# Kernel optimization log

Measured on AMD Instinct MI355X. Metric: run time of the kernel, lower is better.

The kernel has to match this reference:

```python
import jax, jax.numpy as jnp
import numpy as np


def setup_inputs() -> dict:
    key = jax.random.key(0)
    k1, k2, k3, k4 = jax.random.split(key, 4)
    B, N, F, H, O = 4, 2048, 256, 8, 256
    nodes = jax.random.normal(k1, (B, N, F), dtype=jnp.float32)
    W_heads = jax.random.normal(k2, (H, F, F), dtype=jnp.float32) * (1.0 / np.sqrt(F))
    W_out = jax.random.normal(k3, (H * F, O), dtype=jnp.float32) * (1.0 / np.sqrt(H * F))
    bias = jax.random.normal(k4, (O,), dtype=jnp.float32) * 0.02
    return {"nodes": nodes, "W_heads": W_heads, "W_out": W_out, "bias": bias}


def reference(nodes, W_heads, W_out, bias):
    # nodes: [B,N,F]; W_heads: [H,F,F]; W_out: [H*F,O]; bias: [O]
    B, N, F = nodes.shape
    H = W_heads.shape[0]
    norm = 1.0 / jnp.sqrt(jnp.asarray(F, dtype=nodes.dtype))
    # per-head bilinear scores: (x @ W_h) @ x^T  -> [B,H,N,N]
    xw = jnp.einsum('bnf,hfg->bhng', nodes, W_heads)
    scores = jnp.einsum('bhng,bmg->bhnm', xw, nodes) * norm
    att = jax.nn.softmax(scores, axis=-1)
    # messages: att @ x (V = input nodes) -> [B,H,N,F]
    msgs = jnp.einsum('bhnm,bmf->bhnf', att, nodes)
    # concat heads along feature axis (head 0 first) -> [B,N,H*F]
    msgs = msgs.transpose(0, 2, 1, 3).reshape(B, N, H * F)
    return jnp.matmul(msgs, W_out) + bias
```

## Files before the change

### kernel.cpp

```cpp
#include <hip/hip_runtime.h>
#include <hip/hip_bf16.h>

#define B_ 4
#define N_ 2048
#define F_ 256
#define H_ 8
#define O_ 256

#define SCALE_QK 0.09016844005556021f

typedef __attribute__((ext_vector_type(8))) short short8;
typedef __attribute__((ext_vector_type(4))) short s16x4;
typedef __attribute__((ext_vector_type(4))) float f32x4;
typedef __attribute__((ext_vector_type(4))) unsigned int u32x4;

static __device__ __forceinline__ float bf2f(short u) {
    unsigned int x = ((unsigned int)(unsigned short)u) << 16;
    return __builtin_bit_cast(float, x);
}
static __device__ __forceinline__ short f2bf(float f) {
    unsigned int x = __builtin_bit_cast(unsigned int, f);
    unsigned int lsb = (x >> 16) & 1u;
    x += 0x7fffu + lsb;
    return (short)(x >> 16);
}
static __device__ __forceinline__ unsigned int pkbf(float a, float b) {
    return (unsigned int)(unsigned short)f2bf(a) |
           ((unsigned int)(unsigned short)f2bf(b) << 16);
}

static __device__ __forceinline__ void gld16(const short* g, short* l) {
    __builtin_amdgcn_global_load_lds(
        (const __attribute__((address_space(1))) void*)g,
        (__attribute__((address_space(3))) void*)l, 16, 0, 0);
}

__global__ __launch_bounds__(256) void cvtT_kernel(const float* __restrict__ src,
                                                   short* __restrict__ dstT,
                                                   short* __restrict__ dst2,
                                                   int R, int C) {
    __shared__ short tile[32][33];
    src  += (size_t)blockIdx.z * R * C;
    dstT += (size_t)blockIdx.z * R * C;
    if (dst2) dst2 += (size_t)blockIdx.z * R * C;
    int tx = threadIdx.x, ty = threadIdx.y;
    int c0 = blockIdx.x * 32, r0 = blockIdx.y * 32;
#pragma unroll
    for (int j = 0; j < 4; j++) {
        int r = r0 + ty + j * 8;
        short v = f2bf(src[(size_t)r * C + c0 + tx]);
        tile[ty + j * 8][tx] = v;
        if (dst2) dst2[(size_t)r * C + c0 + tx] = v;
    }
    __syncthreads();
#pragma unroll
    for (int j = 0; j < 4; j++) {
        int c = c0 + ty + j * 8;
        dstT[(size_t)c * R + r0 + tx] = tile[tx][ty + j * 8];
    }
}

__global__ __launch_bounds__(256) void cvt_kernel(const float* __restrict__ src,
                                                  short* __restrict__ dst, int n) {
    int i = blockIdx.x * 256 + threadIdx.x;
    if (i < n) dst[i] = f2bf(src[i]);
}

template <int NCT>
__device__ __forceinline__ void gemm64_bt(const short* __restrict__ A, int lda,
                                          const short* __restrict__ Bt, int ldb,
                                          float* __restrict__ C, int ldc,
                                          int K, const short* __restrict__ bias) {
    __shared__ short sA[64][72];
    __shared__ short sB[NCT * 16][72];
    int tid = threadIdx.x;
    int w = tid >> 6, l = tid & 63, lq = l & 15, quad = l >> 4;
    f32x4 acc[NCT];
#pragma unroll
    for (int i = 0; i < NCT; i++) acc[i] = (f32x4)(0.f);

    for (int kb = 0; kb < K; kb += 64) {
        __syncthreads();
#pragma unroll
        for (int i = 0; i < 2; i++) {
            int idx = tid + i * 256; int r = idx >> 3, c = (idx & 7) * 8;
            *(short8*)&sA[r][c] = *(const short8*)&A[(size_t)r * lda + kb + c];
        }
#pragma unroll
        for (int i = 0; i < NCT / 2; i++) {
            int idx = tid + i * 256; int r = idx >> 3, c = (idx & 7) * 8;
            *(short8*)&sB[r][c] = *(const short8*)&Bt[(size_t)r * ldb + kb + c];
        }
        __syncthreads();
#pragma unroll
        for (int kk = 0; kk < 2; kk++) {
            short8 af = *(const short8*)&sA[w * 16 + lq][kk * 32 + quad * 8];
#pragma unroll
            for (int ct = 0; ct < NCT; ct++) {
                short8 bf = *(const short8*)&sB[ct * 16 + lq][kk * 32 + quad * 8];
                acc[ct] = __builtin_amdgcn_mfma_f32_16x16x32_bf16(af, bf, acc[ct], 0, 0, 0);
            }
        }
    }
#pragma unroll
    for (int ct = 0; ct < NCT; ct++) {
        int col = ct * 16 + lq;
        float bv = bias ? bf2f(bias[col]) : 0.f;
#pragma unroll
        for (int r = 0; r < 4; r++) {
            int row = w * 16 + quad * 4 + r;
            C[(size_t)row * ldc + col] = acc[ct][r] + bv;
        }
    }
}

__global__ __launch_bounds__(256) void out_kernel(const short* __restrict__ msgs,
                                                  const short* __restrict__ WoutT,
                                                  const short* __restrict__ bias,
                                                  float* __restrict__ out) {
    int mt = blockIdx.x, nt = blockIdx.y;
    gemm64_bt<4>(msgs + (size_t)mt * 64 * (H_ * F_), H_ * F_,
                 WoutT + (size_t)nt * 64 * (H_ * F_), H_ * F_,
                 out + (size_t)mt * 64 * O_ + nt * 64, O_,
                 H_ * F_, bias + nt * 64);
}


#define STAGE_KV(KT, KVF, KVTF) do {                                         \
    _Pragma("unroll")                                                        \
    for (int i_ = 0; i_ < 4; i_++) {                                         \
        int rk_ = w * 8 + i_ * 2 + (l >> 5);                                 \
        int bk_ = (l & 31) ^ (rk_ & 31);                                     \
        gld16(&Xb[(size_t)((KT) * 64 + rk_) * F_ + bk_ * 8],                 \
              &KVF[(w * 8 + i_ * 2) * 256]);                                 \
        int rt_ = w * 32 + i_ * 8 + (l >> 3);                                \
        int bt_ = (l & 7) ^ (rt_ & 7);                                       \
        gld16(&XTb[(size_t)rt_ * N_ + (KT) * 64 + bt_ * 8],                  \
              &KVTF[(w * 32 + i_ * 8) * 64]);                                \
    }                                                                        \
} while (0)

#define COMPUTE_KT(KVF, KVTF) do {                                           \
    f32x4 sacc[4];                                                           \
    _Pragma("unroll")                                                        \
    for (int ct = 0; ct < 4; ct++) sacc[ct] = (f32x4)(0.f);                  \
    __builtin_amdgcn_s_setprio(1);                                           \
    _Pragma("unroll")                                                        \
    for (int kk = 0; kk < 8; kk++) {                                         \
        _Pragma("unroll")                                                    \
        for (int ct = 0; ct < 4; ct++) {                                     \
            int arow = ct * 16 + lq;                                         \
            int ab = (kk * 4 + quad) ^ (arow & 31);                          \
            short8 af = *(const short8*)&KVF[arow * 256 + ab * 8];           \
            sacc[ct] = __builtin_amdgcn_mfma_f32_16x16x32_bf16(af, aq[kk], sacc[ct], 0, 0, 0); \
        }                                                                    \
    }                                                                        \
    __builtin_amdgcn_s_setprio(0);                                           \
    float mx = -INFINITY;                                                    \
    _Pragma("unroll")                                                        \
    for (int ct = 0; ct < 4; ct++)                                           \
        _Pragma("unroll")                                                    \
        for (int r_ = 0; r_ < 4; r_++) mx = fmaxf(mx, sacc[ct][r_]);         \
    mx = fmaxf(mx, __shfl_xor(mx, 16));                                      \
    mx = fmaxf(mx, __shfl_xor(mx, 32));                                      \
    float mn = fmaxf(m_q, mx);                                               \
    float alpha = exp2f(m_q - mn);                                           \
    m_q = mn;                                                                \
    float pv[4][4]; float s_ = 0.f;                                          \
    _Pragma("unroll")                                                        \
    for (int ct = 0; ct < 4; ct++)                                           \
        _Pragma("unroll")                                                    \
        for (int r_ = 0; r_ < 4; r_++) {                                     \
            pv[ct][r_] = exp2f(sacc[ct][r_] - mn);                           \
            s_ += pv[ct][r_];                                                \
        }                                                                    \
    s_ += __shfl_xor(s_, 16);                                                \
    s_ += __shfl_xor(s_, 32);                                                \
    l_q = l_q * alpha + s_;                                                  \
    if (!__all(alpha == 1.0f)) {                                             \
        _Pragma("unroll")                                                    \
        for (int ct = 0; ct < 16; ct++)                                      \
            _Pragma("unroll")                                                \
            for (int r_ = 0; r_ < 4; r_++) oacc[ct][r_] *= alpha;            \
    }                                                                        \
    unsigned int w2[4][2];                                                   \
    _Pragma("unroll")                                                        \
    for (int ct = 0; ct < 4; ct++) {                                         \
        w2[ct][0] = pkbf(pv[ct][0], pv[ct][1]);                              \
        w2[ct][1] = pkbf(pv[ct][2], pv[ct][3]);                              \
    }                                                                        \
    int sl0 = (2 * (quad & 1)) * 16 + lq;                                    \
    int sl1 = sl0 + 16;                                                      \
    bool hi = (quad >> 1) != 0;                                              \
    short8 pfrag[2];                                                         \
    _Pragma("unroll")                                                        \
    for (int kk = 0; kk < 2; kk++) {                                         \
        unsigned int u0 = __shfl((int)w2[2 * kk][0], sl0);                   \
        unsigned int u1 = __shfl((int)w2[2 * kk][1], sl0);                   \
        unsigned int u2 = __shfl((int)w2[2 * kk][0], sl1);                   \
        unsigned int u3 = __shfl((int)w2[2 * kk][1], sl1);                   \
        unsigned int v0 = __shfl((int)w2[2 * kk + 1][0], sl0);               \
        unsigned int v1 = __shfl((int)w2[2 * kk + 1][1], sl0);               \
        unsigned int v2 = __shfl((int)w2[2 * kk + 1][0], sl1);               \
        unsigned int v3 = __shfl((int)w2[2 * kk + 1][1], sl1);               \
        u32x4 pk = { hi ? v0 : u0, hi ? v1 : u1, hi ? v2 : u2, hi ? v3 : u3 }; \
        pfrag[kk] = __builtin_bit_cast(short8, pk);                          \
    }                                                                        \
    __builtin_amdgcn_s_setprio(1);                                           \
    _Pragma("unroll")                                                        \
    for (int ct = 0; ct < 16; ct++) {                                        \
        int arow = ct * 16 + lq;                                             \
        short8 a0 = *(const short8*)&KVTF[arow * 64 + ((quad) ^ (arow & 7)) * 8]; \
        short8 a1 = *(const short8*)&KVTF[arow * 64 + ((4 + quad) ^ (arow & 7)) * 8]; \
        oacc[ct] = __builtin_amdgcn_mfma_f32_16x16x32_bf16(a0, pfrag[0], oacc[ct], 0, 0, 0); \
        oacc[ct] = __builtin_amdgcn_mfma_f32_16x16x32_bf16(a1, pfrag[1], oacc[ct], 0, 0, 0); \
    }                                                                        \
    __builtin_amdgcn_s_setprio(0);                                           \
} while (0)

__global__ __launch_bounds__(512) void attn_kernel(const short* __restrict__ X,
                                                   const short* __restrict__ WhT,
                                                   const short* __restrict__ XT,
                                                   short* __restrict__ msgs) {
    __shared__ short kvfA[64 * 256];
    __shared__ short kvfB[64 * 256];
    __shared__ short kvTfA[256 * 64];
    __shared__ short kvTfB[256 * 64];

    int qt = blockIdx.x, bh = blockIdx.y, b = bh >> 3, h = bh & 7;
    int tid = threadIdx.x, w = tid >> 6, l = tid & 63, lq = l & 15, quad = l >> 4;
    int q0 = qt * 128;

    const short* Xb  = X  + (size_t)b * N_ * F_;
    const short* XTb = XT + (size_t)b * F_ * N_;
    const short* Whh = WhT + (size_t)h * F_ * F_;

    f32x4 oacc[16];
    short8 aq[8];

#pragma unroll
    for (int i = 0; i < 16; i++) oacc[i] = (f32x4)(0.f);
    {
        short* xdst = (w < 4) ? kvfA : kvfB;
        int wl = w & 3;
#pragma unroll
        for (int i = 0; i < 8; i++) {
            int r = wl * 16 + i * 2 + (l >> 5);
            int bb = (l & 31) ^ (r & 31);
            gld16(&Xb[(size_t)(q0 + ((w >> 2) * 64) + r) * F_ + bb * 8],
                  &xdst[(wl * 16 + i * 2) * 256]);
        }
    }
    const short* xsrc = (w < 4) ? kvfA : kvfB;
#pragma unroll 1
    for (int kb = 0; kb < 4; kb++) {
        __syncthreads();
#pragma unroll
        for (int i = 0; i < 4; i++) {
            int rt = w * 32 + i * 8 + (l >> 3);
            int bt = (l & 7) ^ (rt & 7);
            gld16(&Whh[(size_t)rt * F_ + kb * 64 + bt * 8], &kvTfA[(w * 32 + i * 8) * 64]);
        }
        __syncthreads();
#pragma unroll
        for (int kk = 0; kk < 2; kk++) {
            int arow = (w & 3) * 16 + lq;
            int ab = (kb * 8 + kk * 4 + quad) ^ (arow & 31);
            short8 af = *(const short8*)&xsrc[arow * 256 + ab * 8];
#pragma unroll
            for (int ct = 0; ct < 16; ct++) {
                int brow = ct * 16 + lq;
                int bb = (kk * 4 + quad) ^ (brow & 7);
                short8 bf = *(const short8*)&kvTfA[brow * 64 + bb * 8];
                oacc[ct] = __builtin_amdgcn_mfma_f32_16x16x32_bf16(af, bf, oacc[ct], 0, 0, 0);
            }
        }
    }
    __syncthreads();
    {
        short* qdst = (w < 4) ? kvTfA : kvTfB;
#pragma unroll
        for (int ct = 0; ct < 16; ct++) {
#pragma unroll
            for (int r = 0; r < 4; r++) {
                int row = (w & 3) * 16 + quad * 4 + r;
                int col = ct * 16 + lq;
                int pb = (col >> 3) ^ (row & 31);
                qdst[row * 256 + pb * 8 + (col & 7)] = f2bf(oacc[ct][r] * SCALE_QK);
            }
        }
        __syncthreads();
#pragma unroll
        for (int kk = 0; kk < 8; kk++) {
            int row = (w & 3) * 16 + lq;
            int ab = (kk * 4 + quad) ^ (row & 31);
            aq[kk] = *(const short8*)&qdst[row * 256 + ab * 8];
        }
    }
    __syncthreads();

#pragma unroll
    for (int i = 0; i < 16; i++) oacc[i] = (f32x4)(0.f);
    float m_q = -INFINITY, l_q = 0.f;

    STAGE_KV(0, kvfA, kvTfA);

#pragma unroll 1
    for (int kt = 0; kt < 32; kt++) {
        const short* KVF  = (kt & 1) ? kvfB  : kvfA;
        const short* KVTF = (kt & 1) ? kvTfB : kvTfA;
        short* nKVF  = (kt & 1) ? kvfA  : kvfB;
        short* nKVTF = (kt & 1) ? kvTfA : kvTfB;
        STAGE_KV((kt + 1) & 31, nKVF, nKVTF);
        asm volatile("s_waitcnt vmcnt(8)" ::: "memory");
        __builtin_amdgcn_sched_barrier(0);
        __builtin_amdgcn_s_barrier();
        __builtin_amdgcn_sched_barrier(0);
        COMPUTE_KT(KVF, KVTF);
        __builtin_amdgcn_sched_barrier(0);
        __builtin_amdgcn_s_barrier();
        __builtin_amdgcn_sched_barrier(0);
    }

    float inv = 1.f / l_q;
    short* Mout = msgs + (size_t)(b * N_ + q0 + w * 16 + lq) * (H_ * F_) + h * F_;
#pragma unroll
    for (int ct = 0; ct < 16; ct++) {
        s16x4 v4 = { f2bf(oacc[ct][0] * inv), f2bf(oacc[ct][1] * inv),
                     f2bf(oacc[ct][2] * inv), f2bf(oacc[ct][3] * inv) };
        *(s16x4*)&Mout[ct * 16 + quad * 4] = v4;
    }
}

extern "C" void kernel_launch(void* const* d_in, const int* in_sizes, int n_in,
                              void* d_out, int out_size, void* d_ws, size_t ws_size,
                              hipStream_t stream) {
    const float* nodes = (const float*)d_in[0];
    const float* Wh    = (const float*)d_in[1];
    const float* Wout  = (const float*)d_in[2];
    const float* bias  = (const float*)d_in[3];
    float* out = (float*)d_out;

    char* ws = (char*)d_ws;
    short* msgs   = (short*)(ws);
    short* WhT    = (short*)(ws + 33554432);
    short* WoutT  = (short*)(ws + 34603008);
    short* XT     = (short*)(ws + 35651584);
    short* Xbf    = (short*)(ws + 39845888);
    short* biasbf = (short*)(ws + 44040192);

    dim3 tblk(32, 8, 1);
    hipLaunchKernelGGL(cvtT_kernel, dim3(8, 8, 8),  tblk, 0, stream, Wh,    WhT,   (short*)nullptr, 256,  256);
    hipLaunchKernelGGL(cvtT_kernel, dim3(8, 64, 1), tblk, 0, stream, Wout,  WoutT, (short*)nullptr, 2048, 256);
    hipLaunchKernelGGL(cvtT_kernel, dim3(8, 64, 4), tblk, 0, stream, nodes, XT,    Xbf,             2048, 256);
    hipLaunchKernelGGL(cvt_kernel,  dim3(1),    dim3(256), 0, stream, bias, biasbf, 256);

    hipLaunchKernelGGL(attn_kernel, dim3(16, 32), dim3(512), 0, stream, Xbf, WhT, XT, msgs);
    hipLaunchKernelGGL(out_kernel,  dim3(128, 4), dim3(256), 0, stream, msgs, WoutT, biasbf, out);
}
```

Measured before the change: 343.5 us.

## Lazy softmax rescaling, hardware bf16 pack, and unrolled double-buffer loop

The online softmax now skips the running-max update and the rescale of the output accumulator unless some row's max grows by more than 8 (in log2 units). The deferred rescale is intended to be safe as long as exponents stay bounded. Manual round-to-nearest bf16 packing is replaced by the v_cvt_pk_bf16_f32 instruction. The KV loop is unrolled by two with fixed A/B buffers and plain __syncthreads, dropping the explicit vmcnt waits and sched barriers. This removes pointer selection and per-iteration rescale work, but it relies on __syncthreads to drain the async global-to-LDS loads, which changes how loads overlap with compute.

```diff
diff --git a/kernel.cpp b/kernel.cpp
--- a/kernel.cpp
+++ b/kernel.cpp
@@ -24,9 +24,10 @@
     x += 0x7fffu + lsb;
     return (short)(x >> 16);
 }
-static __device__ __forceinline__ unsigned int pkbf(float a, float b) {
-    return (unsigned int)(unsigned short)f2bf(a) |
-           ((unsigned int)(unsigned short)f2bf(b) << 16);
+static __device__ __forceinline__ unsigned int cvtpk(float a, float b) {
+    unsigned int r;
+    asm("v_cvt_pk_bf16_f32 %0, %1, %2" : "=v"(r) : "v"(a), "v"(b));
+    return r;
 }
 
 static __device__ __forceinline__ void gld16(const short* g, short* l) {
@@ -163,31 +164,32 @@
         for (int r_ = 0; r_ < 4; r_++) mx = fmaxf(mx, sacc[ct][r_]);         \
     mx = fmaxf(mx, __shfl_xor(mx, 16));                                      \
     mx = fmaxf(mx, __shfl_xor(mx, 32));                                      \
-    float mn = fmaxf(m_q, mx);                                               \
-    float alpha = exp2f(m_q - mn);                                           \
-    m_q = mn;                                                                \
+    if (!__all(mx - m_q <= 8.0f)) {                \
+        float mn = fmaxf(m_q, mx);                                           \
+        float alpha = exp2f(m_q - mn);                                       \
+        m_q = mn;                                                            \
+        l_q *= alpha;                                                        \
+        _Pragma("unroll")                                                    \
+        for (int ct = 0; ct < 16; ct++)                                      \
+            _Pragma("unroll")                                                \
+            for (int r_ = 0; r_ < 4; r_++) oacc[ct][r_] *= alpha;            \
+    }                                                                        \
     float pv[4][4]; float s_ = 0.f;                                          \
     _Pragma("unroll")                                                        \
     for (int ct = 0; ct < 4; ct++)                                           \
         _Pragma("unroll")                                                    \
         for (int r_ = 0; r_ < 4; r_++) {                                     \
-            pv[ct][r_] = exp2f(sacc[ct][r_] - mn);                           \
+            pv[ct][r_] = exp2f(sacc[ct][r_] - m_q);                          \
             s_ += pv[ct][r_];                                                \
         }                                                                    \
     s_ += __shfl_xor(s_, 16);                                                \
     s_ += __shfl_xor(s_, 32);                                                \
-    l_q = l_q * alpha + s_;                                                  \
-    if (!__all(alpha == 1.0f)) {                                             \
-        _Pragma("unroll")                                                    \
-        for (int ct = 0; ct < 16; ct++)                                      \
-            _Pragma("unroll")                                                \
-            for (int r_ = 0; r_ < 4; r_++) oacc[ct][r_] *= alpha;            \
-    }                                                                        \
+    l_q += s_;                                                               \
     unsigned int w2[4][2];                                                   \
     _Pragma("unroll")                                                        \
     for (int ct = 0; ct < 4; ct++) {                                         \
-        w2[ct][0] = pkbf(pv[ct][0], pv[ct][1]);                              \
-        w2[ct][1] = pkbf(pv[ct][2], pv[ct][3]);                              \
+        w2[ct][0] = cvtpk(pv[ct][0], pv[ct][1]);                             \
+        w2[ct][1] = cvtpk(pv[ct][2], pv[ct][3]);                             \
     }                                                                        \
     int sl0 = (2 * (quad & 1)) * 16 + lq;                                    \
     int sl1 = sl0 + 16;                                                      \
@@ -304,22 +306,16 @@
     float m_q = -INFINITY, l_q = 0.f;
 
     STAGE_KV(0, kvfA, kvTfA);
+    __syncthreads();
 
 #pragma unroll 1
-    for (int kt = 0; kt < 32; kt++) {
-        const short* KVF  = (kt & 1) ? kvfB  : kvfA;
-        const short* KVTF = (kt & 1) ? kvTfB : kvTfA;
-        short* nKVF  = (kt & 1) ? kvfA  : kvfB;
-        short* nKVTF = (kt & 1) ? kvTfA : kvTfB;
-        STAGE_KV((kt + 1) & 31, nKVF, nKVTF);
-        asm volatile("s_waitcnt vmcnt(8)" ::: "memory");
-        __builtin_amdgcn_sched_barrier(0);
-        __builtin_amdgcn_s_barrier();
-        __builtin_amdgcn_sched_barrier(0);
-        COMPUTE_KT(KVF, KVTF);
-        __builtin_amdgcn_sched_barrier(0);
-        __builtin_amdgcn_s_barrier();
-        __builtin_amdgcn_sched_barrier(0);
+    for (int kt2 = 0; kt2 < 16; kt2++) {
+        STAGE_KV(2 * kt2 + 1, kvfB, kvTfB);
+        COMPUTE_KT(kvfA, kvTfA);
+        __syncthreads();
+        STAGE_KV((2 * kt2 + 2) & 31, kvfA, kvTfA);
+        COMPUTE_KT(kvfB, kvTfB);
+        __syncthreads();
     }
 
     float inv = 1.f / l_q;
```

New measurement: 289.2 us. 1.19x faster.
